# Kernel optimization log

Hardware: AMD Instinct MI355X
Metric: run time of the kernel (lower is better)

Reference implementation:

```python
import jax, jax.numpy as jnp
import numpy as np
import math

D_MODEL = 1024
NUM_HEADS = 16
HEAD_DIM = D_MODEL // NUM_HEADS
REPETITIONS = 3
NEG = -10000.0


def setup_inputs() -> dict:
    key = jax.random.key(0)
    ks = jax.random.split(key, 5)
    B, S = 2, 2048
    x = jax.random.normal(ks[0], (B, S, D_MODEL), dtype=jnp.float32)
    Wqkv_w = jax.random.normal(ks[1], (3 * D_MODEL, D_MODEL), dtype=jnp.float32) * (1.0 / math.sqrt(D_MODEL))
    Wqkv_b = jax.random.normal(ks[2], (3 * D_MODEL,), dtype=jnp.float32) * 0.02
    out_w = jax.random.normal(ks[3], (D_MODEL, D_MODEL), dtype=jnp.float32) * (1.0 / math.sqrt(D_MODEL))
    out_b = jax.random.normal(ks[4], (D_MODEL,), dtype=jnp.float32) * 0.02
    return {"x": x, "Wqkv_w": Wqkv_w, "Wqkv_b": Wqkv_b, "out_w": out_w, "out_b": out_b}


def _self_attention(q, k, v, mask):
    # q,k,v: (B,S,H,D); mask: (S,S) additive causal (-10000 above diagonal)
    scale = 1.0 / math.sqrt(q.shape[-1])
    scores = jnp.einsum('bthd,bshd->bhts', q, k * scale) + mask  # (B,H,S,S)
    attn = jax.nn.softmax(scores, axis=-1)
    return jnp.einsum('bhts,bshd->bthd', attn, v)  # (B,S,H,D)


def reference(x, Wqkv_w, Wqkv_b, out_w, out_b):
    B, S, _ = x.shape
    qkv = x @ Wqkv_w.T + Wqkv_b                       # (B,S,3*D_MODEL)
    qkv = qkv.reshape(B, S, 3, NUM_HEADS, HEAD_DIM)
    q, k, v = qkv[:, :, 0], qkv[:, :, 1], qkv[:, :, 2]
    mask = jnp.triu(jnp.full((S, S), NEG, dtype=x.dtype), 1)
    context = _self_attention(q, k, v, mask)
    # recurrent re-attention: rep_dim == 'q' -> query replaced by previous context
    for _ in range(REPETITIONS - 1):
        context = _self_attention(context, k, v, mask)
    out = context.reshape(B, S, D_MODEL) @ out_w.T + out_b
    return out
```

## Files before the change

kernel.cpp:

```cpp
#include <hip/hip_runtime.h>


#define D_MODEL 1024
#define NHEADS  16
#define HD      64
#define SEQ     2048
#define BATCH   2
#define NROWS   (BATCH*SEQ)
#define NQKV    (3*D_MODEL)
#define SCL2F   0.1803368801111601f
#define MASK2   (-14426.950408889634f)

typedef __bf16 bf16x8 __attribute__((ext_vector_type(8)));
typedef float  f32x4  __attribute__((ext_vector_type(4)));
typedef unsigned short us8 __attribute__((ext_vector_type(8)));
typedef unsigned short us4 __attribute__((ext_vector_type(4)));
typedef short  s16x4  __attribute__((ext_vector_type(4)));

__device__ __forceinline__ unsigned short f2bf(float f) {
  unsigned int u = __float_as_uint(f);
  u = (u + 0x7fffu + ((u >> 16) & 1u)) >> 16;
  return (unsigned short)u;
}

union Pack8 { us8 v; unsigned short e[8]; };
union Pack4 { us4 v; unsigned short e[4]; };

__device__ __forceinline__ us8 cvt8(const float4 &a, const float4 &b) {
  Pack8 p;
  p.e[0]=f2bf(a.x); p.e[1]=f2bf(a.y); p.e[2]=f2bf(a.z); p.e[3]=f2bf(a.w);
  p.e[4]=f2bf(b.x); p.e[5]=f2bf(b.y); p.e[6]=f2bf(b.z); p.e[7]=f2bf(b.w);
  return p.v;
}

__device__ __forceinline__ void gl_lds16(const unsigned short* g, unsigned short* l) {
  __builtin_amdgcn_global_load_lds(
      (const __attribute__((address_space(1))) unsigned int*)g,
      (__attribute__((address_space(3))) unsigned int*)l, 16, 0, 0);
}

#define CVT_N1 (NROWS*D_MODEL)
#define CVT_N2 (NQKV*D_MODEL)
#define CVT_N3 (D_MODEL*D_MODEL)

__global__ __launch_bounds__(256) void cvt_all(
    const float* __restrict__ x, const float* __restrict__ wq,
    const float* __restrict__ ow,
    unsigned short* __restrict__ xb, unsigned short* __restrict__ wqb,
    unsigned short* __restrict__ owb)
{
  size_t i = ((size_t)blockIdx.x * 256 + threadIdx.x) * 8;
  const float* src; unsigned short* dst; size_t off;
  if (i < CVT_N1)                { src = x;  dst = xb;  off = i; }
  else if (i < CVT_N1 + CVT_N2)  { src = wq; dst = wqb; off = i - CVT_N1; }
  else                           { src = ow; dst = owb; off = i - CVT_N1 - CVT_N2; }
  float4 a = *(const float4*)(src + off);
  float4 b = *(const float4*)(src + off + 4);
  *(us8*)(dst + off) = cvt8(a, b);
}

__global__ __launch_bounds__(256) void qkv_gemm(
    const unsigned short* __restrict__ xb, const unsigned short* __restrict__ wqb,
    const float* __restrict__ bias,
    unsigned short* __restrict__ q, unsigned short* __restrict__ k,
    unsigned short* __restrict__ vT)
{
  __shared__ __align__(16) unsigned short As[128*64];
  __shared__ __align__(16) unsigned short Bs[128*64];
  const int tid = threadIdx.x;
  const int m0 = blockIdx.y * 128, n0 = blockIdx.x * 128;
  const int wave = tid >> 6, lane = tid & 63;
  const int wm = (wave >> 1) * 64, wn = (wave & 1) * 64;
  const int lrow = lane & 15, quad = lane >> 4;

  const int dr = lane >> 3;
  const int pg = lane & 7;
  const int sg = (pg ^ dr) * 8;
  const unsigned short* gA[4]; const unsigned short* gB[4];
  unsigned short *lA[4], *lB[4];
  #pragma unroll
  for (int i = 0; i < 4; i++) {
    int c = wave*4 + i;
    gA[i] = xb  + (size_t)(m0 + c*8 + dr) * D_MODEL + sg;
    gB[i] = wqb + (size_t)(n0 + c*8 + dr) * D_MODEL + sg;
    lA[i] = &As[c*512];
    lB[i] = &Bs[c*512];
  }
  const int px0 = (quad ^ (lrow & 7)) * 8;
  const int px1 = ((quad + 4) ^ (lrow & 7)) * 8;

  f32x4 acc[4][4];
  #pragma unroll
  for (int i = 0; i < 4; i++)
    #pragma unroll
    for (int j = 0; j < 4; j++) acc[i][j] = (f32x4){0.f,0.f,0.f,0.f};

  for (int k0 = 0; k0 < D_MODEL; k0 += 64) {
    __syncthreads();
    #pragma unroll
    for (int i = 0; i < 4; i++) { gl_lds16(gA[i] + k0, lA[i]); gl_lds16(gB[i] + k0, lB[i]); }
    __syncthreads();
    bf16x8 af[4][2], bfr[4][2];
    #pragma unroll
    for (int mf = 0; mf < 4; mf++) {
      int row = wm + mf*16 + lrow;
      af[mf][0] = *(const bf16x8*)&As[row*64 + px0];
      af[mf][1] = *(const bf16x8*)&As[row*64 + px1];
    }
    #pragma unroll
    for (int nb = 0; nb < 4; nb++) {
      int row = wn + nb*16 + lrow;
      bfr[nb][0] = *(const bf16x8*)&Bs[row*64 + px0];
      bfr[nb][1] = *(const bf16x8*)&Bs[row*64 + px1];
    }
    #pragma unroll
    for (int h = 0; h < 2; h++)
      #pragma unroll
      for (int mf = 0; mf < 4; mf++)
        #pragma unroll
        for (int nb = 0; nb < 4; nb++)
          acc[mf][nb] = __builtin_amdgcn_mfma_f32_16x16x32_bf16(af[mf][h], bfr[nb][h], acc[mf][nb], 0, 0, 0);
  }

  #pragma unroll
  for (int mf = 0; mf < 4; mf++) {
    #pragma unroll
    for (int nb = 0; nb < 4; nb++) {
      int n = n0 + wn + nb*16 + lrow;
      int which = n >> 10;
      int h  = (n >> 6) & 15;
      int hd = n & 63;
      int mb = m0 + wm + mf*16 + quad*4;
      int b  = mb >> 11;
      int s  = mb & 2047;
      float bi = bias[n];
      if (which == 2) {
        Pack4 p4;
        #pragma unroll
        for (int r = 0; r < 4; r++) p4.e[r] = f2bf(acc[mf][nb][r] + bi);
        *(us4*)&vT[((size_t)((b*NHEADS + h)*HD + hd))*SEQ + s] = p4.v;
      } else {
        unsigned short* dst = (which == 0) ? q : k;
        float scl = (which == 0) ? SCL2F : 1.0f;
        #pragma unroll
        for (int r = 0; r < 4; r++)
          dst[(size_t)((b*NHEADS + h)*SEQ + s + r)*HD + hd] = f2bf((acc[mf][nb][r] + bi) * scl);
      }
    }
  }
}

#define LDQ 72

__global__ __launch_bounds__(512, 2) void attn3(
    const unsigned short* __restrict__ qg,
    const unsigned short* __restrict__ kg,
    const unsigned short* __restrict__ vTg,
    unsigned short* __restrict__ ctx)
{
  __shared__ __align__(16) unsigned short Ks[4][64*LDQ];
  __shared__ __align__(16) unsigned short Vs[4][64*LDQ];
  unsigned short* QC = &Vs[0][0];

  const int tid  = threadIdx.x;
  const int w    = tid >> 6, lane = tid & 63;
  const int lrow = lane & 15, quad = lane >> 4;
  const int bh  = blockIdx.x;
  const int qt8 = blockIdx.y;
  const unsigned short* qbase = qg  + (size_t)bh * SEQ * HD;
  const unsigned short* kbase = kg  + (size_t)bh * SEQ * HD;
  const unsigned short* vbase = vTg + (size_t)bh * HD * SEQ;
  unsigned short* cbase = ctx + (size_t)bh * SEQ * HD;

  const int srow = tid >> 3;
  const int sco  = (tid & 7) * 8;
  const int qrow = tid >> 1, qc0 = (tid & 1) * 32;

  {
    const unsigned short* src = qbase + (size_t)(qt8*256 + qrow)*HD + qc0;
    *(uint4*)&QC[qrow*LDQ + qc0]      = *(const uint4*)src;
    *(uint4*)&QC[qrow*LDQ + qc0 + 8]  = *(const uint4*)(src + 8);
    *(uint4*)&QC[qrow*LDQ + qc0 + 16] = *(const uint4*)(src + 16);
    *(uint4*)&QC[qrow*LDQ + qc0 + 24] = *(const uint4*)(src + 24);
  }
  __syncthreads();

  bf16x8 qb[2][2];
  #pragma unroll
  for (int qgi = 0; qgi < 2; qgi++) {
    qb[qgi][0] = *(const bf16x8*)&QC[(w*32 + qgi*16 + lrow)*LDQ + quad*8];
    qb[qgi][1] = *(const bf16x8*)&QC[(w*32 + qgi*16 + lrow)*LDQ + 32 + quad*8];
  }
  __syncthreads();

  const int qwbase = qt8*256 + w*32;
  const int npair = 2*qt8 + 2;

  for (int rep = 0; rep < 3; ++rep) {
    f32x4 od[2][4];
    #pragma unroll
    for (int qgi = 0; qgi < 2; qgi++)
      #pragma unroll
      for (int df = 0; df < 4; df++) od[qgi][df] = (f32x4){0.f,0.f,0.f,0.f};
    float ls[2] = {0.f, 0.f};

    uint4 ka, kb, va, vb;
    {
      const unsigned short* ks = kbase + (size_t)srow*HD + sco;
      ka = *(const uint4*)ks;  kb = *(const uint4*)(ks + 64*HD);
      const unsigned short* vs = vbase + (size_t)srow*SEQ + sco;
      va = *(const uint4*)vs;  vb = *(const uint4*)(vs + 64);
    }

    for (int t = 0; t < npair; ++t) {
      const int pb = (t & 1) * 2;
      *(uint4*)&Ks[pb][srow*LDQ + sco]   = ka;
      *(uint4*)&Ks[pb+1][srow*LDQ + sco] = kb;
      *(uint4*)&Vs[pb][srow*LDQ + sco]   = va;
      *(uint4*)&Vs[pb+1][srow*LDQ + sco] = vb;
      if (t + 1 < npair) {
        const unsigned short* ks = kbase + (size_t)((2*t+2)*64 + srow)*HD + sco;
        ka = *(const uint4*)ks;  kb = *(const uint4*)(ks + 64*HD);
        const unsigned short* vs = vbase + (size_t)srow*SEQ + (2*t+2)*64 + sco;
        va = *(const uint4*)vs;  vb = *(const uint4*)(vs + 64);
      }
      __syncthreads();

      #pragma unroll
      for (int half = 0; half < 2; ++half) {
        const int bb = pb + half;
        const int sbase = (2*t + half) * 64;
        if (sbase > qwbase + 31) continue;
        f32x4 sc[2][4];
        __builtin_amdgcn_s_setprio(1);
        #pragma unroll
        for (int sf = 0; sf < 4; sf++) {
          bf16x8 a0 = *(const bf16x8*)&Ks[bb][(sf*16 + lrow)*LDQ + quad*8];
          bf16x8 a1 = *(const bf16x8*)&Ks[bb][(sf*16 + lrow)*LDQ + 32 + quad*8];
          f32x4 z0 = (f32x4){0.f,0.f,0.f,0.f}, z1 = (f32x4){0.f,0.f,0.f,0.f};
          z0 = __builtin_amdgcn_mfma_f32_16x16x32_bf16(a0, qb[0][0], z0, 0, 0, 0);
          z1 = __builtin_amdgcn_mfma_f32_16x16x32_bf16(a0, qb[1][0], z1, 0, 0, 0);
          z0 = __builtin_amdgcn_mfma_f32_16x16x32_bf16(a1, qb[0][1], z0, 0, 0, 0);
          z1 = __builtin_amdgcn_mfma_f32_16x16x32_bf16(a1, qb[1][1], z1, 0, 0, 0);
          sc[0][sf] = z0; sc[1][sf] = z1;
        }
        __builtin_amdgcn_s_setprio(0);
        if (sbase + 63 > qwbase) {
          #pragma unroll
          for (int qgi = 0; qgi < 2; qgi++) {
            int ql = qwbase + qgi*16 + lrow;
            #pragma unroll
            for (int sf = 0; sf < 4; sf++)
              #pragma unroll
              for (int r = 0; r < 4; r++)
                if (sbase + sf*16 + quad*4 + r > ql) sc[qgi][sf][r] += MASK2;
          }
        }
        s16x4 pf[2][4];
        #pragma unroll
        for (int qgi = 0; qgi < 2; qgi++) {
          float lp = 0.f;
          #pragma unroll
          for (int sf = 0; sf < 4; sf++) {
            Pack4 pk;
            #pragma unroll
            for (int r = 0; r < 4; r++) {
              float pe = __builtin_amdgcn_exp2f(sc[qgi][sf][r]);
              lp += pe;
              pk.e[r] = __builtin_bit_cast(unsigned short, (__bf16)pe);
            }
            pf[qgi][sf] = __builtin_bit_cast(s16x4, pk.v);
          }
          ls[qgi] += lp;
        }
        __builtin_amdgcn_s_setprio(1);
        #pragma unroll
        for (int df = 0; df < 4; df++) {
          s16x4 v0 = *(const s16x4*)&Vs[bb][(df*16 + lrow)*LDQ +  0 + quad*4];
          s16x4 v1 = *(const s16x4*)&Vs[bb][(df*16 + lrow)*LDQ + 16 + quad*4];
          s16x4 v2 = *(const s16x4*)&Vs[bb][(df*16 + lrow)*LDQ + 32 + quad*4];
          s16x4 v3 = *(const s16x4*)&Vs[bb][(df*16 + lrow)*LDQ + 48 + quad*4];
          od[0][df] = __builtin_amdgcn_mfma_f32_16x16x16bf16_1k(v0, pf[0][0], od[0][df], 0, 0, 0);
          od[1][df] = __builtin_amdgcn_mfma_f32_16x16x16bf16_1k(v0, pf[1][0], od[1][df], 0, 0, 0);
          od[0][df] = __builtin_amdgcn_mfma_f32_16x16x16bf16_1k(v1, pf[0][1], od[0][df], 0, 0, 0);
          od[1][df] = __builtin_amdgcn_mfma_f32_16x16x16bf16_1k(v1, pf[1][1], od[1][df], 0, 0, 0);
          od[0][df] = __builtin_amdgcn_mfma_f32_16x16x16bf16_1k(v2, pf[0][2], od[0][df], 0, 0, 0);
          od[1][df] = __builtin_amdgcn_mfma_f32_16x16x16bf16_1k(v2, pf[1][2], od[1][df], 0, 0, 0);
          od[0][df] = __builtin_amdgcn_mfma_f32_16x16x16bf16_1k(v3, pf[0][3], od[0][df], 0, 0, 0);
          od[1][df] = __builtin_amdgcn_mfma_f32_16x16x16bf16_1k(v3, pf[1][3], od[1][df], 0, 0, 0);
        }
        __builtin_amdgcn_s_setprio(0);
      }
    }

    #pragma unroll
    for (int qgi = 0; qgi < 2; qgi++) {
      ls[qgi] += __shfl_xor(ls[qgi], 16);
      ls[qgi] += __shfl_xor(ls[qgi], 32);
    }

    __syncthreads();
    #pragma unroll
    for (int qgi = 0; qgi < 2; qgi++) {
      float f = ((rep < 2) ? SCL2F : 1.0f) / ls[qgi];
      #pragma unroll
      for (int df = 0; df < 4; df++) {
        Pack4 pk;
        #pragma unroll
        for (int r = 0; r < 4; r++)
          pk.e[r] = __builtin_bit_cast(unsigned short, (__bf16)(od[qgi][df][r] * f));
        *(us4*)&QC[(w*32 + qgi*16 + lrow)*LDQ + df*16 + quad*4] = pk.v;
      }
    }
    __syncthreads();
    if (rep < 2) {
      #pragma unroll
      for (int qgi = 0; qgi < 2; qgi++) {
        qb[qgi][0] = *(const bf16x8*)&QC[(w*32 + qgi*16 + lrow)*LDQ + quad*8];
        qb[qgi][1] = *(const bf16x8*)&QC[(w*32 + qgi*16 + lrow)*LDQ + 32 + quad*8];
      }
      __syncthreads();
    }
  }

  {
    unsigned short* dst = cbase + (size_t)(qt8*256 + qrow)*HD + qc0;
    *(uint4*)dst        = *(const uint4*)&QC[qrow*LDQ + qc0];
    *(uint4*)(dst + 8)  = *(const uint4*)&QC[qrow*LDQ + qc0 + 8];
    *(uint4*)(dst + 16) = *(const uint4*)&QC[qrow*LDQ + qc0 + 16];
    *(uint4*)(dst + 24) = *(const uint4*)&QC[qrow*LDQ + qc0 + 24];
  }
}

__global__ __launch_bounds__(256) void out_gemm(
    const unsigned short* __restrict__ ctx, const unsigned short* __restrict__ owb,
    const float* __restrict__ bias, float* __restrict__ out)
{
  __shared__ __align__(16) unsigned short As[128*64];
  __shared__ __align__(16) unsigned short Bs[64*64];
  const int tid = threadIdx.x;
  const int m0 = blockIdx.y * 128, n0 = blockIdx.x * 64;
  const int wave = tid >> 6, lane = tid & 63;
  const int wm = (wave >> 1) * 64, wn = (wave & 1) * 32;
  const int lrow = lane & 15, quad = lane >> 4;

  const int dr = lane >> 3, pg = lane & 7;
  const int sg = (pg ^ dr) * 8;
  size_t aoff[4]; unsigned short* lA[4];
  #pragma unroll
  for (int i = 0; i < 4; i++) {
    int c = wave*4 + i;
    int row = m0 + c*8 + dr;
    aoff[i] = ((size_t)((row >> 11)*NHEADS)*SEQ + (row & 2047))*HD + sg;
    lA[i] = &As[c*512];
  }
  const unsigned short* gB[2]; unsigned short* lB[2];
  #pragma unroll
  for (int j = 0; j < 2; j++) {
    int c = wave*2 + j;
    gB[j] = owb + (size_t)(n0 + c*8 + dr) * D_MODEL + sg;
    lB[j] = &Bs[c*512];
  }
  const int px0 = (quad ^ (lrow & 7)) * 8;
  const int px1 = ((quad + 4) ^ (lrow & 7)) * 8;

  f32x4 acc[4][2];
  #pragma unroll
  for (int i = 0; i < 4; i++)
    #pragma unroll
    for (int j = 0; j < 2; j++) acc[i][j] = (f32x4){0.f,0.f,0.f,0.f};

  for (int k0 = 0; k0 < D_MODEL; k0 += 64) {
    size_t hoff = (size_t)(k0 >> 6) * SEQ * HD;
    __syncthreads();
    #pragma unroll
    for (int i = 0; i < 4; i++) gl_lds16(ctx + aoff[i] + hoff, lA[i]);
    #pragma unroll
    for (int j = 0; j < 2; j++) gl_lds16(gB[j] + k0, lB[j]);
    __syncthreads();
    bf16x8 af[4][2], bfr[2][2];
    #pragma unroll
    for (int mf = 0; mf < 4; mf++) {
      int row = wm + mf*16 + lrow;
      af[mf][0] = *(const bf16x8*)&As[row*64 + px0];
      af[mf][1] = *(const bf16x8*)&As[row*64 + px1];
    }
    #pragma unroll
    for (int nb = 0; nb < 2; nb++) {
      int row = wn + nb*16 + lrow;
      bfr[nb][0] = *(const bf16x8*)&Bs[row*64 + px0];
      bfr[nb][1] = *(const bf16x8*)&Bs[row*64 + px1];
    }
    #pragma unroll
    for (int h = 0; h < 2; h++)
      #pragma unroll
      for (int mf = 0; mf < 4; mf++)
        #pragma unroll
        for (int nb = 0; nb < 2; nb++)
          acc[mf][nb] = __builtin_amdgcn_mfma_f32_16x16x32_bf16(af[mf][h], bfr[nb][h], acc[mf][nb], 0, 0, 0);
  }

  #pragma unroll
  for (int mf = 0; mf < 4; mf++) {
    #pragma unroll
    for (int nb = 0; nb < 2; nb++) {
      #pragma unroll
      for (int r = 0; r < 4; r++) {
        int mm = m0 + wm + mf*16 + quad*4 + r;
        int n  = n0 + wn + nb*16 + lrow;
        out[(size_t)mm * D_MODEL + n] = acc[mf][nb][r] + bias[n];
      }
    }
  }
}

extern "C" void kernel_launch(void* const* d_in, const int* in_sizes, int n_in,
                              void* d_out, int out_size, void* d_ws, size_t ws_size,
                              hipStream_t stream) {
  (void)in_sizes; (void)n_in; (void)out_size; (void)ws_size;
  const float* x      = (const float*)d_in[0];
  const float* Wqkv_w = (const float*)d_in[1];
  const float* Wqkv_b = (const float*)d_in[2];
  const float* out_w  = (const float*)d_in[3];
  const float* out_b  = (const float*)d_in[4];
  float* out = (float*)d_out;

  unsigned short* ws = (unsigned short*)d_ws;
  unsigned short* xb  = ws;
  unsigned short* wqb = ws + CVT_N1;
  unsigned short* owb = ws + CVT_N1 + CVT_N2;
  unsigned short* q   = ws + CVT_N1 + CVT_N2 + CVT_N3;
  unsigned short* k   = q + (size_t)NROWS*D_MODEL;
  unsigned short* vT  = k + (size_t)NROWS*D_MODEL;
  unsigned short* ctx = xb;

  cvt_all<<<(CVT_N1+CVT_N2+CVT_N3)/(256*8), 256, 0, stream>>>(x, Wqkv_w, out_w, xb, wqb, owb);
  qkv_gemm<<<dim3(NQKV/128, NROWS/128), 256, 0, stream>>>(xb, wqb, Wqkv_b, q, k, vT);
  attn3<<<dim3(BATCH*NHEADS, 8), 512, 0, stream>>>(q, k, vT, ctx);
  out_gemm<<<dim3(D_MODEL/64, NROWS/128), 256, 0, stream>>>(ctx, owb, out_b, out);
}
```

Measured before the change: 262.0 us.

## Split KV across wave halves in attention with 128-row query tiles and reduction

Each attention block now handles a 128-row query tile instead of 256. Its 8 waves split into two halves, each processing one of the two 64-key tiles in every pair. Partial outputs and row sums from the second half are reduced through shared memory before normalisation. The grid doubles, query tiles are remapped so work is balanced under the causal mask, and launch bounds request more resident blocks. The aim is to fix triangular load imbalance and raise occupancy. The cost is an extra shared-memory reduction and extra barriers at each repetition.

```diff
diff --git a/kernel.cpp b/kernel.cpp
--- a/kernel.cpp
+++ b/kernel.cpp
@@ -152,7 +152,7 @@
 
 #define LDQ 72
 
-__global__ __launch_bounds__(512, 2) void attn3(
+__global__ __launch_bounds__(512, 4) void attn3(
     const unsigned short* __restrict__ qg,
     const unsigned short* __restrict__ kg,
     const unsigned short* __restrict__ vTg,
@@ -161,12 +161,17 @@
   __shared__ __align__(16) unsigned short Ks[4][64*LDQ];
   __shared__ __align__(16) unsigned short Vs[4][64*LDQ];
   unsigned short* QC = &Vs[0][0];
+  float* scr = (float*)&Ks[0][0];
 
   const int tid  = threadIdx.x;
   const int w    = tid >> 6, lane = tid & 63;
   const int lrow = lane & 15, quad = lane >> 4;
-  const int bh  = blockIdx.x;
-  const int qt8 = blockIdx.y;
+  const int wq = w & 3;
+  const int hf = w >> 2;
+  const int bh = blockIdx.x;
+  const int yy = blockIdx.y;
+  const int base = (blockIdx.x + yy) & 7;
+  const int qt = (yy < 8) ? base : (15 - base);
   const unsigned short* qbase = qg  + (size_t)bh * SEQ * HD;
   const unsigned short* kbase = kg  + (size_t)bh * SEQ * HD;
   const unsigned short* vbase = vTg + (size_t)bh * HD * SEQ;
@@ -174,27 +179,25 @@
 
   const int srow = tid >> 3;
   const int sco  = (tid & 7) * 8;
-  const int qrow = tid >> 1, qc0 = (tid & 1) * 32;
+  const int qrow = tid >> 2, qc0 = (tid & 3) * 16;
 
   {
-    const unsigned short* src = qbase + (size_t)(qt8*256 + qrow)*HD + qc0;
-    *(uint4*)&QC[qrow*LDQ + qc0]      = *(const uint4*)src;
-    *(uint4*)&QC[qrow*LDQ + qc0 + 8]  = *(const uint4*)(src + 8);
-    *(uint4*)&QC[qrow*LDQ + qc0 + 16] = *(const uint4*)(src + 16);
-    *(uint4*)&QC[qrow*LDQ + qc0 + 24] = *(const uint4*)(src + 24);
+    const unsigned short* src = qbase + (size_t)(qt*128 + qrow)*HD + qc0;
+    *(uint4*)&QC[qrow*LDQ + qc0]     = *(const uint4*)src;
+    *(uint4*)&QC[qrow*LDQ + qc0 + 8] = *(const uint4*)(src + 8);
   }
   __syncthreads();
 
   bf16x8 qb[2][2];
   #pragma unroll
   for (int qgi = 0; qgi < 2; qgi++) {
-    qb[qgi][0] = *(const bf16x8*)&QC[(w*32 + qgi*16 + lrow)*LDQ + quad*8];
-    qb[qgi][1] = *(const bf16x8*)&QC[(w*32 + qgi*16 + lrow)*LDQ + 32 + quad*8];
+    qb[qgi][0] = *(const bf16x8*)&QC[(wq*32 + qgi*16 + lrow)*LDQ + quad*8];
+    qb[qgi][1] = *(const bf16x8*)&QC[(wq*32 + qgi*16 + lrow)*LDQ + 32 + quad*8];
   }
   __syncthreads();
 
-  const int qwbase = qt8*256 + w*32;
-  const int npair = 2*qt8 + 2;
+  const int qwbase = qt*128 + wq*32;
+  const int npair = qt + 1;
 
   for (int rep = 0; rep < 3; ++rep) {
     f32x4 od[2][4];
@@ -226,109 +229,122 @@
       }
       __syncthreads();
 
-      #pragma unroll
-      for (int half = 0; half < 2; ++half) {
-        const int bb = pb + half;
-        const int sbase = (2*t + half) * 64;
-        if (sbase > qwbase + 31) continue;
-        f32x4 sc[2][4];
-        __builtin_amdgcn_s_setprio(1);
+      const int bb = pb + hf;
+      const int sbase = (2*t + hf) * 64;
+      if (sbase > qwbase + 31) continue;
+      f32x4 sc[2][4];
+      __builtin_amdgcn_s_setprio(1);
+      #pragma unroll
+      for (int sf = 0; sf < 4; sf++) {
+        bf16x8 a0 = *(const bf16x8*)&Ks[bb][(sf*16 + lrow)*LDQ + quad*8];
+        bf16x8 a1 = *(const bf16x8*)&Ks[bb][(sf*16 + lrow)*LDQ + 32 + quad*8];
+        f32x4 z0 = (f32x4){0.f,0.f,0.f,0.f}, z1 = (f32x4){0.f,0.f,0.f,0.f};
+        z0 = __builtin_amdgcn_mfma_f32_16x16x32_bf16(a0, qb[0][0], z0, 0, 0, 0);
+        z1 = __builtin_amdgcn_mfma_f32_16x16x32_bf16(a0, qb[1][0], z1, 0, 0, 0);
+        z0 = __builtin_amdgcn_mfma_f32_16x16x32_bf16(a1, qb[0][1], z0, 0, 0, 0);
+        z1 = __builtin_amdgcn_mfma_f32_16x16x32_bf16(a1, qb[1][1], z1, 0, 0, 0);
+        sc[0][sf] = z0; sc[1][sf] = z1;
+      }
+      __builtin_amdgcn_s_setprio(0);
+      if (sbase + 63 > qwbase) {
+        #pragma unroll
+        for (int qgi = 0; qgi < 2; qgi++) {
+          int ql = qwbase + qgi*16 + lrow;
+          #pragma unroll
+          for (int sf = 0; sf < 4; sf++)
+            #pragma unroll
+            for (int r = 0; r < 4; r++)
+              if (sbase + sf*16 + quad*4 + r > ql) sc[qgi][sf][r] += MASK2;
+        }
+      }
+      s16x4 pf[2][4];
+      #pragma unroll
+      for (int qgi = 0; qgi < 2; qgi++) {
+        float lp = 0.f;
         #pragma unroll
         for (int sf = 0; sf < 4; sf++) {
-          bf16x8 a0 = *(const bf16x8*)&Ks[bb][(sf*16 + lrow)*LDQ + quad*8];
-          bf16x8 a1 = *(const bf16x8*)&Ks[bb][(sf*16 + lrow)*LDQ + 32 + quad*8];
-          f32x4 z0 = (f32x4){0.f,0.f,0.f,0.f}, z1 = (f32x4){0.f,0.f,0.f,0.f};
-          z0 = __builtin_amdgcn_mfma_f32_16x16x32_bf16(a0, qb[0][0], z0, 0, 0, 0);
-          z1 = __builtin_amdgcn_mfma_f32_16x16x32_bf16(a0, qb[1][0], z1, 0, 0, 0);
-          z0 = __builtin_amdgcn_mfma_f32_16x16x32_bf16(a1, qb[0][1], z0, 0, 0, 0);
-          z1 = __builtin_amdgcn_mfma_f32_16x16x32_bf16(a1, qb[1][1], z1, 0, 0, 0);
-          sc[0][sf] = z0; sc[1][sf] = z1;
+          Pack4 pk;
+          #pragma unroll
+          for (int r = 0; r < 4; r++) {
+            float pe = __builtin_amdgcn_exp2f(sc[qgi][sf][r]);
+            lp += pe;
+            pk.e[r] = __builtin_bit_cast(unsigned short, (__bf16)pe);
+          }
+          pf[qgi][sf] = __builtin_bit_cast(s16x4, pk.v);
         }
-        __builtin_amdgcn_s_setprio(0);
-        if (sbase + 63 > qwbase) {
+        ls[qgi] += lp;
+      }
+      __builtin_amdgcn_s_setprio(1);
+      #pragma unroll
+      for (int df = 0; df < 4; df++) {
+        s16x4 v0 = *(const s16x4*)&Vs[bb][(df*16 + lrow)*LDQ +  0 + quad*4];
+        s16x4 v1 = *(const s16x4*)&Vs[bb][(df*16 + lrow)*LDQ + 16 + quad*4];
+        s16x4 v2 = *(const s16x4*)&Vs[bb][(df*16 + lrow)*LDQ + 32 + quad*4];
+        s16x4 v3 = *(const s16x4*)&Vs[bb][(df*16 + lrow)*LDQ + 48 + quad*4];
+        od[0][df] = __builtin_amdgcn_mfma_f32_16x16x16bf16_1k(v0, pf[0][0], od[0][df], 0, 0, 0);
+        od[1][df] = __builtin_amdgcn_mfma_f32_16x16x16bf16_1k(v0, pf[1][0], od[1][df], 0, 0, 0);
+        od[0][df] = __builtin_amdgcn_mfma_f32_16x16x16bf16_1k(v1, pf[0][1], od[0][df], 0, 0, 0);
+        od[1][df] = __builtin_amdgcn_mfma_f32_16x16x16bf16_1k(v1, pf[1][1], od[1][df], 0, 0, 0);
+        od[0][df] = __builtin_amdgcn_mfma_f32_16x16x16bf16_1k(v2, pf[0][2], od[0][df], 0, 0, 0);
+        od[1][df] = __builtin_amdgcn_mfma_f32_16x16x16bf16_1k(v2, pf[1][2], od[1][df], 0, 0, 0);
+        od[0][df] = __builtin_amdgcn_mfma_f32_16x16x16bf16_1k(v3, pf[0][3], od[0][df], 0, 0, 0);
+        od[1][df] = __builtin_amdgcn_mfma_f32_16x16x16bf16_1k(v3, pf[1][3], od[1][df], 0, 0, 0);
+      }
+      __builtin_amdgcn_s_setprio(0);
+    }
+
+    __syncthreads();
+    if (w >= 4) {
+      float* p = scr + (size_t)(tid - 256) * 36;
+      #pragma unroll
+      for (int qgi = 0; qgi < 2; qgi++)
+        #pragma unroll
+        for (int df = 0; df < 4; df++)
+          *(f32x4*)(p + qgi*16 + df*4) = od[qgi][df];
+      p[32] = ls[0]; p[33] = ls[1];
+    }
+    __syncthreads();
+    if (w < 4) {
+      const float* p = scr + (size_t)tid * 36;
+      #pragma unroll
+      for (int qgi = 0; qgi < 2; qgi++)
+        #pragma unroll
+        for (int df = 0; df < 4; df++)
+          od[qgi][df] += *(const f32x4*)(p + qgi*16 + df*4);
+      ls[0] += p[32]; ls[1] += p[33];
+      #pragma unroll
+      for (int qgi = 0; qgi < 2; qgi++) {
+        ls[qgi] += __shfl_xor(ls[qgi], 16);
+        ls[qgi] += __shfl_xor(ls[qgi], 32);
+      }
+      #pragma unroll
+      for (int qgi = 0; qgi < 2; qgi++) {
+        float f = ((rep < 2) ? SCL2F : 1.0f) / ls[qgi];
+        #pragma unroll
+        for (int df = 0; df < 4; df++) {
+          Pack4 pk;
           #pragma unroll
-          for (int qgi = 0; qgi < 2; qgi++) {
-            int ql = qwbase + qgi*16 + lrow;
-            #pragma unroll
-            for (int sf = 0; sf < 4; sf++)
-              #pragma unroll
-              for (int r = 0; r < 4; r++)
-                if (sbase + sf*16 + quad*4 + r > ql) sc[qgi][sf][r] += MASK2;
-          }
+          for (int r = 0; r < 4; r++)
+            pk.e[r] = __builtin_bit_cast(unsigned short, (__bf16)(od[qgi][df][r] * f));
+          *(us4*)&QC[(wq*32 + qgi*16 + lrow)*LDQ + df*16 + quad*4] = pk.v;
         }
-        s16x4 pf[2][4];
-        #pragma unroll
-        for (int qgi = 0; qgi < 2; qgi++) {
-          float lp = 0.f;
-          #pragma unroll
-          for (int sf = 0; sf < 4; sf++) {
-            Pack4 pk;
-            #pragma unroll
-            for (int r = 0; r < 4; r++) {
-              float pe = __builtin_amdgcn_exp2f(sc[qgi][sf][r]);
-              lp += pe;
-              pk.e[r] = __builtin_bit_cast(unsigned short, (__bf16)pe);
-            }
-            pf[qgi][sf] = __builtin_bit_cast(s16x4, pk.v);
-          }
-          ls[qgi] += lp;
-        }
-        __builtin_amdgcn_s_setprio(1);
-        #pragma unroll
-        for (int df = 0; df < 4; df++) {
-          s16x4 v0 = *(const s16x4*)&Vs[bb][(df*16 + lrow)*LDQ +  0 + quad*4];
-          s16x4 v1 = *(const s16x4*)&Vs[bb][(df*16 + lrow)*LDQ + 16 + quad*4];
-          s16x4 v2 = *(const s16x4*)&Vs[bb][(df*16 + lrow)*LDQ + 32 + quad*4];
-          s16x4 v3 = *(const s16x4*)&Vs[bb][(df*16 + lrow)*LDQ + 48 + quad*4];
-          od[0][df] = __builtin_amdgcn_mfma_f32_16x16x16bf16_1k(v0, pf[0][0], od[0][df], 0, 0, 0);
-          od[1][df] = __builtin_amdgcn_mfma_f32_16x16x16bf16_1k(v0, pf[1][0], od[1][df], 0, 0, 0);
-          od[0][df] = __builtin_amdgcn_mfma_f32_16x16x16bf16_1k(v1, pf[0][1], od[0][df], 0, 0, 0);
-          od[1][df] = __builtin_amdgcn_mfma_f32_16x16x16bf16_1k(v1, pf[1][1], od[1][df], 0, 0, 0);
-          od[0][df] = __builtin_amdgcn_mfma_f32_16x16x16bf16_1k(v2, pf[0][2], od[0][df], 0, 0, 0);
-          od[1][df] = __builtin_amdgcn_mfma_f32_16x16x16bf16_1k(v2, pf[1][2], od[1][df], 0, 0, 0);
-          od[0][df] = __builtin_amdgcn_mfma_f32_16x16x16bf16_1k(v3, pf[0][3], od[0][df], 0, 0, 0);
-          od[1][df] = __builtin_amdgcn_mfma_f32_16x16x16bf16_1k(v3, pf[1][3], od[1][df], 0, 0, 0);
-        }
-        __builtin_amdgcn_s_setprio(0);
-      }
-    }
-
-    #pragma unroll
-    for (int qgi = 0; qgi < 2; qgi++) {
-      ls[qgi] += __shfl_xor(ls[qgi], 16);
-      ls[qgi] += __shfl_xor(ls[qgi], 32);
-    }
-
-    __syncthreads();
-    #pragma unroll
-    for (int qgi = 0; qgi < 2; qgi++) {
-      float f = ((rep < 2) ? SCL2F : 1.0f) / ls[qgi];
-      #pragma unroll
-      for (int df = 0; df < 4; df++) {
-        Pack4 pk;
-        #pragma unroll
-        for (int r = 0; r < 4; r++)
-          pk.e[r] = __builtin_bit_cast(unsigned short, (__bf16)(od[qgi][df][r] * f));
-        *(us4*)&QC[(w*32 + qgi*16 + lrow)*LDQ + df*16 + quad*4] = pk.v;
       }
     }
     __syncthreads();
     if (rep < 2) {
       #pragma unroll
       for (int qgi = 0; qgi < 2; qgi++) {
-        qb[qgi][0] = *(const bf16x8*)&QC[(w*32 + qgi*16 + lrow)*LDQ + quad*8];
-        qb[qgi][1] = *(const bf16x8*)&QC[(w*32 + qgi*16 + lrow)*LDQ + 32 + quad*8];
+        qb[qgi][0] = *(const bf16x8*)&QC[(wq*32 + qgi*16 + lrow)*LDQ + quad*8];
+        qb[qgi][1] = *(const bf16x8*)&QC[(wq*32 + qgi*16 + lrow)*LDQ + 32 + quad*8];
       }
       __syncthreads();
     }
   }
 
   {
-    unsigned short* dst = cbase + (size_t)(qt8*256 + qrow)*HD + qc0;
-    *(uint4*)dst        = *(const uint4*)&QC[qrow*LDQ + qc0];
-    *(uint4*)(dst + 8)  = *(const uint4*)&QC[qrow*LDQ + qc0 + 8];
-    *(uint4*)(dst + 16) = *(const uint4*)&QC[qrow*LDQ + qc0 + 16];
-    *(uint4*)(dst + 24) = *(const uint4*)&QC[qrow*LDQ + qc0 + 24];
+    unsigned short* dst = cbase + (size_t)(qt*128 + qrow)*HD + qc0;
+    *(uint4*)dst       = *(const uint4*)&QC[qrow*LDQ + qc0];
+    *(uint4*)(dst + 8) = *(const uint4*)&QC[qrow*LDQ + qc0 + 8];
   }
 }
 
@@ -436,6 +452,6 @@
 
   cvt_all<<<(CVT_N1+CVT_N2+CVT_N3)/(256*8), 256, 0, stream>>>(x, Wqkv_w, out_w, xb, wqb, owb);
   qkv_gemm<<<dim3(NQKV/128, NROWS/128), 256, 0, stream>>>(xb, wqb, Wqkv_b, q, k, vT);
-  attn3<<<dim3(BATCH*NHEADS, 8), 512, 0, stream>>>(q, k, vT, ctx);
+  attn3<<<dim3(BATCH*NHEADS, SEQ/128), 512, 0, stream>>>(q, k, vT, ctx);
   out_gemm<<<dim3(D_MODEL/64, NROWS/128), 256, 0, stream>>>(ctx, owb, out_b, out);
 }
```

New measurement: 265.8 us. No clear change (+1.5%).
